# Performance work log

Measured on AMD Instinct MI355X. Metric: run time of the kernel, lower is better.

Reference implementation:

```python
import jax, jax.numpy as jnp
import numpy as np

N = 250_000   # total instances
D = 128       # instance latent dim
F = 512       # raw instance feature dim
B = 5000      # number of bags


def setup_inputs() -> dict:
    key = jax.random.key(0)
    ks = jax.random.split(key, 7)
    z_ins = jax.random.normal(ks[0], (N, D), dtype=jnp.float32)
    bag_idx = jnp.sort(jax.random.randint(ks[1], (N,), 0, B, dtype=jnp.int32))
    bag_instances = jax.random.normal(ks[2], (N, F), dtype=jnp.float32)
    instance_mu = jax.random.normal(ks[3], (N, D), dtype=jnp.float32)
    instance_std = jax.random.uniform(ks[4], (N, D), dtype=jnp.float32)
    W = jax.random.normal(ks[5], (D, 1), dtype=jnp.float32) * 0.05
    b = jnp.zeros((1,), dtype=jnp.float32)
    return {"z_ins": z_ins, "bag_idx": bag_idx, "bag_instances": bag_instances,
            "instance_mu": instance_mu, "instance_std": instance_std,
            "W": W, "b": b}


def reference(z_ins, bag_idx, bag_instances, instance_mu, instance_std, W, b):
    # loc_ins = fc_ins(z_ins): [N, 1]
    loc_ins = z_ins @ W + b
    loc = loc_ins[:, 0]  # [N]

    # Segmented max over bags; argmax gather (first max index, matching torch.max).
    seg_max = jax.ops.segment_max(loc, bag_idx, num_segments=B)          # [B]
    is_max = loc == seg_max[bag_idx]                                     # [N]
    cand = jnp.where(is_max, jnp.arange(N, dtype=jnp.int32), N)
    arg = jax.ops.segment_min(cand, bag_idx, num_segments=B)            # [B]
    empty = arg >= N                                                     # bags with no instances stay zero
    arg_c = jnp.minimum(arg, N - 1)

    def gather(x):
        return jnp.where(empty[:, None], jnp.zeros((), x.dtype), x[arg_c])

    M = gather(loc_ins)                       # [B, 1]
    max_z_ins = gather(z_ins)                 # [B, D]
    max_instances = gather(bag_instances)     # [B, F]
    max_instances_mu = gather(instance_mu)    # [B, D]
    max_instances_std = gather(instance_std)  # [B, D]
    return (M, max_instances, max_z_ins, loc_ins, max_instances_mu, max_instances_std)
```

## Files before the change

kernel.cpp:

```cpp
#include <hip/hip_runtime.h>

#define DD 128
#define FF 512
#define BAGS 5000

__device__ __forceinline__ unsigned fkey(float f) {
    unsigned u = __float_as_uint(f);
    return (u & 0x80000000u) ? ~u : (u | 0x80000000u);
}
__device__ __forceinline__ float fkey_inv(unsigned k) {
    unsigned u = (k & 0x80000000u) ? (k & 0x7FFFFFFFu) : ~k;
    return __uint_as_float(u);
}

__global__ __launch_bounds__(256) void loc_seg_kernel(
    const float* __restrict__ z, const int* __restrict__ bag,
    const float* __restrict__ W, const float* __restrict__ b,
    float* __restrict__ loc, unsigned long long* __restrict__ packed, int N)
{
    int tid  = threadIdx.x;
    int lane = tid & 63;
    int wave = tid >> 6;
    int o    = lane & 7;
    int rowslot = lane >> 3;

    long long rowbase = (long long)blockIdx.x * 256 + wave * 64;

    float4 wk[4];
    #pragma unroll
    for (int j = 0; j < 4; ++j) wk[j] = ((const float4*)W)[o + 8 * j];
    float bb = b[0];

    float myloc = 0.f;
    #pragma unroll
    for (int t = 0; t < 8; ++t) {
        long long row = rowbase + t * 8 + rowslot;
        float4 acc = make_float4(0.f, 0.f, 0.f, 0.f);
        if (row < N) {
            const float4* zr = (const float4*)(z + row * DD);
            #pragma unroll
            for (int j = 0; j < 4; ++j) {
                float4 zv = zr[o + 8 * j];
                acc.x = fmaf(zv.x, wk[j].x, acc.x);
                acc.y = fmaf(zv.y, wk[j].y, acc.y);
                acc.z = fmaf(zv.z, wk[j].z, acc.z);
                acc.w = fmaf(zv.w, wk[j].w, acc.w);
            }
        }
        float sd = (acc.x + acc.y) + (acc.z + acc.w);
        sd += __shfl_xor(sd, 1, 64);
        sd += __shfl_xor(sd, 2, 64);
        sd += __shfl_xor(sd, 4, 64);
        float v = __shfl(sd, (lane & 7) * 8, 64);
        if (t == (lane >> 3)) myloc = v;
    }

    long long row = rowbase + lane;
    bool valid = row < N;
    myloc += bb;
    int bl = -1;
    unsigned long long key = 0ull;
    if (valid) {
        loc[row] = myloc;
        bl = bag[row];
        key = ((unsigned long long)fkey(myloc) << 32) | (unsigned)(N - 1 - (int)row);
    }
    #pragma unroll
    for (int off = 1; off <= 32; off <<= 1) {
        int src = lane + off;
        int clamped = src < 64 ? src : lane;
        unsigned long long okey = __shfl(key, clamped, 64);
        int obag = __shfl(bl, clamped, 64);
        if (src < 64 && obag == bl && okey > key) key = okey;
    }
    int pb = __shfl(bl, lane > 0 ? lane - 1 : 0, 64);
    bool head = valid && (lane == 0 || pb != bl);
    if (head) atomicMax(&packed[bl], key);
}

__global__ __launch_bounds__(256) void gather_kernel(
    const float* __restrict__ z, const float* __restrict__ inst,
    const float* __restrict__ mu, const float* __restrict__ stdv,
    const unsigned long long* __restrict__ packed,
    float* __restrict__ oM, float* __restrict__ oInst, float* __restrict__ oZ,
    float* __restrict__ oMu, float* __restrict__ oStd, int N)
{
    int bagi = blockIdx.x;
    unsigned long long p = packed[bagi];
    bool empty = (p == 0ull);
    long long ac = empty ? 0 : (long long)(N - 1 - (int)(unsigned)(p & 0xFFFFFFFFull));
    const float4 zero4 = make_float4(0.f, 0.f, 0.f, 0.f);
    int t = threadIdx.x;
    if (t < 128) {
        float4 v = empty ? zero4 : ((const float4*)(inst + ac * FF))[t];
        ((float4*)(oInst + (long long)bagi * FF))[t] = v;
    } else if (t < 160) {
        int k = t - 128;
        float4 v = empty ? zero4 : ((const float4*)(z + ac * DD))[k];
        ((float4*)(oZ + (long long)bagi * DD))[k] = v;
    } else if (t < 192) {
        int k = t - 160;
        float4 v = empty ? zero4 : ((const float4*)(mu + ac * DD))[k];
        ((float4*)(oMu + (long long)bagi * DD))[k] = v;
    } else if (t < 224) {
        int k = t - 192;
        float4 v = empty ? zero4 : ((const float4*)(stdv + ac * DD))[k];
        ((float4*)(oStd + (long long)bagi * DD))[k] = v;
    } else if (t == 224) {
        oM[bagi] = empty ? 0.f : fkey_inv((unsigned)(p >> 32));
    }
}

extern "C" void kernel_launch(void* const* d_in, const int* in_sizes, int n_in,
                              void* d_out, int out_size, void* d_ws, size_t ws_size,
                              hipStream_t stream) {
    const float* z    = (const float*)d_in[0];
    const int*   bag  = (const int*)d_in[1];
    const float* inst = (const float*)d_in[2];
    const float* mu   = (const float*)d_in[3];
    const float* stdv = (const float*)d_in[4];
    const float* W    = (const float*)d_in[5];
    const float* b    = (const float*)d_in[6];
    int N = in_sizes[1];

    float* out = (float*)d_out;
    long long off_inst = BAGS;
    long long off_z    = off_inst + (long long)BAGS * FF;
    long long off_loc  = off_z    + (long long)BAGS * DD;
    long long off_mu   = off_loc  + N;
    long long off_std  = off_mu   + (long long)BAGS * DD;

    unsigned long long* packed = (unsigned long long*)d_ws;
    float* loc = out + off_loc;

    hipMemsetAsync(packed, 0, BAGS * sizeof(unsigned long long), stream);
    int blocks = (N + 255) / 256;
    loc_seg_kernel<<<blocks, 256, 0, stream>>>(z, bag, W, b, loc, packed, N);
    gather_kernel<<<BAGS, 256, 0, stream>>>(z, inst, mu, stdv, packed,
                                            out, out + off_inst, out + off_z,
                                            out + off_mu, out + off_std, N);
}
```

Baseline: 40.24 us.

## Fuse segment argmax and gather into a single kernel with last-arriver completion

Merges the loc/segment-max kernel and the gather kernel into one launch. Bags that lie wholly inside a block are reduced in shared memory and gathered immediately. Bags that span blocks are tracked with atomic start/end/count counters, so the last contributing block does the gather. Empty bags are zeroed inline by the thread that sees the gap in bag indices. This removes the second launch and the global round trip on the argmax keys, but adds atomics, fences and serial per-lane fallback paths.

```diff
diff --git a/kernel.cpp b/kernel.cpp
--- a/kernel.cpp
+++ b/kernel.cpp
@@ -3,6 +3,7 @@
 #define DD 128
 #define FF 512
 #define BAGS 5000
+#define TASK_CAP 32
 
 __device__ __forceinline__ unsigned fkey(float f) {
     unsigned u = __float_as_uint(f);
@@ -13,28 +14,72 @@
     return __uint_as_float(u);
 }
 
-__global__ __launch_bounds__(256) void loc_seg_kernel(
+__device__ void zero_bag(int bg, float* oM, float* oInst, float* oZ,
+                         float* oMu, float* oStd) {
+    oM[bg] = 0.f;
+    const float4 z4 = make_float4(0.f, 0.f, 0.f, 0.f);
+    float4* pi = (float4*)(oInst + (long long)bg * FF);
+    for (int k = 0; k < FF / 4; ++k) pi[k] = z4;
+    float4* pz = (float4*)(oZ + (long long)bg * DD);
+    float4* pm = (float4*)(oMu + (long long)bg * DD);
+    float4* ps = (float4*)(oStd + (long long)bg * DD);
+    for (int k = 0; k < DD / 4; ++k) { pz[k] = z4; pm[k] = z4; ps[k] = z4; }
+}
+
+__device__ void lane_gather(int bg, unsigned long long p, int N,
+                            const float* z, const float* inst, const float* mu,
+                            const float* stdv, float* oM, float* oInst,
+                            float* oZ, float* oMu, float* oStd) {
+    long long ac = N - 1 - (int)(unsigned)(p & 0xFFFFFFFFull);
+    oM[bg] = fkey_inv((unsigned)(p >> 32));
+    for (int k = 0; k < FF; ++k) oInst[(long long)bg * FF + k] = inst[ac * FF + k];
+    for (int k = 0; k < DD; ++k) {
+        oZ[(long long)bg * DD + k]  = z[ac * DD + k];
+        oMu[(long long)bg * DD + k] = mu[ac * DD + k];
+        oStd[(long long)bg * DD + k] = stdv[ac * DD + k];
+    }
+}
+
+__global__ __launch_bounds__(256) void fused_kernel(
     const float* __restrict__ z, const int* __restrict__ bag,
-    const float* __restrict__ W, const float* __restrict__ b,
-    float* __restrict__ loc, unsigned long long* __restrict__ packed, int N)
+    const float* __restrict__ inst, const float* __restrict__ mu,
+    const float* __restrict__ stdv, const float* __restrict__ W,
+    const float* __restrict__ bptr,
+    float* __restrict__ oM, float* __restrict__ oInst, float* __restrict__ oZ,
+    float* __restrict__ oMu, float* __restrict__ oStd, float* __restrict__ loc,
+    unsigned long long* __restrict__ packed, unsigned* __restrict__ bagstart,
+    unsigned* __restrict__ bagend, unsigned* __restrict__ done, int N)
 {
+    __shared__ unsigned long long keyA[256];
+    __shared__ int bagA[256];
+    __shared__ int s_prev, s_next, s_ntask;
+    __shared__ int taskBag[TASK_CAP];
+    __shared__ unsigned long long taskKey[TASK_CAP];
+
     int tid  = threadIdx.x;
     int lane = tid & 63;
     int wave = tid >> 6;
-    int o    = lane & 7;
+    long long rowbase = (long long)blockIdx.x * 256;
+
+    if (tid == 0) {
+        s_prev = (rowbase > 0) ? bag[rowbase - 1] : -1;
+        long long nr = rowbase + 256;
+        s_next = (nr < N) ? bag[nr] : BAGS;
+        s_ntask = 0;
+    }
+
+    int o = lane & 7;
     int rowslot = lane >> 3;
-
-    long long rowbase = (long long)blockIdx.x * 256 + wave * 64;
-
+    long long wbase = rowbase + (long long)wave * 64;
     float4 wk[4];
     #pragma unroll
     for (int j = 0; j < 4; ++j) wk[j] = ((const float4*)W)[o + 8 * j];
-    float bb = b[0];
+    float bb = bptr[0];
 
     float myloc = 0.f;
     #pragma unroll
     for (int t = 0; t < 8; ++t) {
-        long long row = rowbase + t * 8 + rowslot;
+        long long row = wbase + t * 8 + rowslot;
         float4 acc = make_float4(0.f, 0.f, 0.f, 0.f);
         if (row < N) {
             const float4* zr = (const float4*)(z + row * DD);
@@ -55,59 +100,102 @@
         if (t == (lane >> 3)) myloc = v;
     }
 
-    long long row = rowbase + lane;
-    bool valid = row < N;
+    long long myrow = wbase + lane;
+    bool valid = myrow < N;
     myloc += bb;
-    int bl = -1;
-    unsigned long long key = 0ull;
+    int mybag = BAGS;
+    unsigned long long mykey = 0ull;
     if (valid) {
-        loc[row] = myloc;
-        bl = bag[row];
-        key = ((unsigned long long)fkey(myloc) << 32) | (unsigned)(N - 1 - (int)row);
-    }
+        loc[myrow] = myloc;
+        mybag = bag[myrow];
+        mykey = ((unsigned long long)fkey(myloc) << 32) | (unsigned)(N - 1 - (int)myrow);
+    }
+
     #pragma unroll
     for (int off = 1; off <= 32; off <<= 1) {
         int src = lane + off;
-        int clamped = src < 64 ? src : lane;
-        unsigned long long okey = __shfl(key, clamped, 64);
-        int obag = __shfl(bl, clamped, 64);
-        if (src < 64 && obag == bl && okey > key) key = okey;
-    }
-    int pb = __shfl(bl, lane > 0 ? lane - 1 : 0, 64);
-    bool head = valid && (lane == 0 || pb != bl);
-    if (head) atomicMax(&packed[bl], key);
-}
-
-__global__ __launch_bounds__(256) void gather_kernel(
-    const float* __restrict__ z, const float* __restrict__ inst,
-    const float* __restrict__ mu, const float* __restrict__ stdv,
-    const unsigned long long* __restrict__ packed,
-    float* __restrict__ oM, float* __restrict__ oInst, float* __restrict__ oZ,
-    float* __restrict__ oMu, float* __restrict__ oStd, int N)
-{
-    int bagi = blockIdx.x;
-    unsigned long long p = packed[bagi];
-    bool empty = (p == 0ull);
-    long long ac = empty ? 0 : (long long)(N - 1 - (int)(unsigned)(p & 0xFFFFFFFFull));
-    const float4 zero4 = make_float4(0.f, 0.f, 0.f, 0.f);
-    int t = threadIdx.x;
-    if (t < 128) {
-        float4 v = empty ? zero4 : ((const float4*)(inst + ac * FF))[t];
-        ((float4*)(oInst + (long long)bagi * FF))[t] = v;
-    } else if (t < 160) {
-        int k = t - 128;
-        float4 v = empty ? zero4 : ((const float4*)(z + ac * DD))[k];
-        ((float4*)(oZ + (long long)bagi * DD))[k] = v;
-    } else if (t < 192) {
-        int k = t - 160;
-        float4 v = empty ? zero4 : ((const float4*)(mu + ac * DD))[k];
-        ((float4*)(oMu + (long long)bagi * DD))[k] = v;
-    } else if (t < 224) {
-        int k = t - 192;
-        float4 v = empty ? zero4 : ((const float4*)(stdv + ac * DD))[k];
-        ((float4*)(oStd + (long long)bagi * DD))[k] = v;
-    } else if (t == 224) {
-        oM[bagi] = empty ? 0.f : fkey_inv((unsigned)(p >> 32));
+        int cl = src < 64 ? src : lane;
+        unsigned long long ok = __shfl(mykey, cl, 64);
+        int ob = __shfl(mybag, cl, 64);
+        if (src < 64 && ob == mybag && ok > mykey) mykey = ok;
+    }
+    keyA[tid] = mykey;
+    bagA[tid] = mybag;
+    __syncthreads();
+
+    int pb = (tid == 0) ? s_prev : bagA[tid - 1];
+    bool rep = valid && (tid == 0 || pb != mybag);
+
+    if (rep) {
+        for (int w2 = wave + 1; w2 < 4; ++w2) {
+            if (bagA[w2 * 64] != mybag) break;
+            unsigned long long ok = keyA[w2 * 64];
+            if (ok > mykey) mykey = ok;
+        }
+    }
+
+    {
+        int hi = (mybag < BAGS ? mybag : BAGS) - 1;
+        for (int bg = pb + 1; bg <= hi; ++bg)
+            zero_bag(bg, oM, oInst, oZ, oMu, oStd);
+        if (valid && tid == 255 && rowbase + 256 >= N && mybag < BAGS - 1)
+            for (int bg = mybag + 1; bg < BAGS; ++bg)
+                zero_bag(bg, oM, oInst, oZ, oMu, oStd);
+    }
+
+    if (rep) {
+        int lastbagblk = bagA[255];
+        bool gfirst = (tid > 0) || (mybag != s_prev);
+        bool reaches_end = (mybag == lastbagblk);
+        bool glast = !reaches_end || (s_next != mybag);
+
+        if (gfirst && glast) {
+            int idx = atomicAdd(&s_ntask, 1);
+            if (idx < TASK_CAP) { taskBag[idx] = mybag; taskKey[idx] = mykey; }
+            else lane_gather(mybag, mykey, N, z, inst, mu, stdv, oM, oInst, oZ, oMu, oStd);
+        } else {
+            int t2 = tid;
+            while (t2 + 1 < 256 && bagA[t2 + 1] == mybag) ++t2;
+            int C = t2 - tid + 1;
+            if (gfirst) atomicMax(&bagstart[mybag], (unsigned)(N - (int)(rowbase + tid)));
+            if (glast)  atomicMax(&bagend[mybag],   (unsigned)(rowbase + t2 + 1));
+            atomicMax(&packed[mybag], mykey);
+            __threadfence();
+            unsigned total = atomicAdd(&done[mybag], (unsigned)C) + (unsigned)C;
+            __threadfence();
+            unsigned bs = atomicMax(&bagstart[mybag], 0u);
+            unsigned be = atomicMax(&bagend[mybag], 0u);
+            if (bs != 0u && be != 0u &&
+                (long long)total == (long long)be + (long long)bs - (long long)N) {
+                unsigned long long K = atomicMax(&packed[mybag], 0ull);
+                int idx = atomicAdd(&s_ntask, 1);
+                if (idx < TASK_CAP) { taskBag[idx] = mybag; taskKey[idx] = K; }
+                else lane_gather(mybag, K, N, z, inst, mu, stdv, oM, oInst, oZ, oMu, oStd);
+            }
+        }
+    }
+    __syncthreads();
+
+    int nt = s_ntask; if (nt > TASK_CAP) nt = TASK_CAP;
+    for (int q = 0; q < nt; ++q) {
+        int bg = taskBag[q];
+        unsigned long long p = taskKey[q];
+        long long ac = N - 1 - (int)(unsigned)(p & 0xFFFFFFFFull);
+        int t = tid;
+        if (t < 128) {
+            ((float4*)(oInst + (long long)bg * FF))[t] = ((const float4*)(inst + ac * FF))[t];
+        } else if (t < 160) {
+            int k = t - 128;
+            ((float4*)(oZ + (long long)bg * DD))[k] = ((const float4*)(z + ac * DD))[k];
+        } else if (t < 192) {
+            int k = t - 160;
+            ((float4*)(oMu + (long long)bg * DD))[k] = ((const float4*)(mu + ac * DD))[k];
+        } else if (t < 224) {
+            int k = t - 192;
+            ((float4*)(oStd + (long long)bg * DD))[k] = ((const float4*)(stdv + ac * DD))[k];
+        } else if (t == 224) {
+            oM[bg] = fkey_inv((unsigned)(p >> 32));
+        }
     }
 }
 
@@ -131,12 +219,15 @@
     long long off_std  = off_mu   + (long long)BAGS * DD;
 
     unsigned long long* packed = (unsigned long long*)d_ws;
-    float* loc = out + off_loc;
-
-    hipMemsetAsync(packed, 0, BAGS * sizeof(unsigned long long), stream);
+    unsigned* bagstart = (unsigned*)((char*)d_ws + BAGS * 8);
+    unsigned* bagend   = (unsigned*)((char*)d_ws + BAGS * 8 + BAGS * 4);
+    unsigned* done     = (unsigned*)((char*)d_ws + BAGS * 8 + BAGS * 8);
+
+    hipMemsetAsync(d_ws, 0, BAGS * 20, stream);
     int blocks = (N + 255) / 256;
-    loc_seg_kernel<<<blocks, 256, 0, stream>>>(z, bag, W, b, loc, packed, N);
-    gather_kernel<<<BAGS, 256, 0, stream>>>(z, inst, mu, stdv, packed,
-                                            out, out + off_inst, out + off_z,
-                                            out + off_mu, out + off_std, N);
-}
+    fused_kernel<<<blocks, 256, 0, stream>>>(
+        z, bag, inst, mu, stdv, W, b,
+        out, out + off_inst, out + off_z, out + off_mu, out + off_std,
+        out + off_loc,
+        packed, bagstart, bagend, done, N);
+}
```

Measured after the change: 123.0 us. +205.7%, slower.

## Replace atomic segment max with segment start offsets and per-bag reduction

Applied to the files above, without the earlier changes.

The first kernel no longer runs a wave-level segmented scan and atomicMax on packed keys. It writes segment start offsets from boundaries in the sorted bag indices. The gather kernel then reads each bag's range, reduces the argmax over loc with one wave, and copies the rows. This drops the memset launch and the atomics, at the cost of re-reading loc per bag and a serial wave reduction before the copy. It relies on bag_idx being sorted.

```diff
diff --git a/kernel.cpp b/kernel.cpp
--- a/kernel.cpp
+++ b/kernel.cpp
@@ -13,10 +13,10 @@
     return __uint_as_float(u);
 }
 
-__global__ __launch_bounds__(256) void loc_seg_kernel(
+__global__ __launch_bounds__(256) void loc_kernel(
     const float* __restrict__ z, const int* __restrict__ bag,
     const float* __restrict__ W, const float* __restrict__ b,
-    float* __restrict__ loc, unsigned long long* __restrict__ packed, int N)
+    float* __restrict__ loc, int* __restrict__ start, int N)
 {
     int tid  = threadIdx.x;
     int lane = tid & 63;
@@ -24,7 +24,7 @@
     int o    = lane & 7;
     int rowslot = lane >> 3;
 
-    long long rowbase = (long long)blockIdx.x * 256 + wave * 64;
+    long long wbase = (long long)blockIdx.x * 256 + wave * 64;
 
     float4 wk[4];
     #pragma unroll
@@ -34,7 +34,7 @@
     float myloc = 0.f;
     #pragma unroll
     for (int t = 0; t < 8; ++t) {
-        long long row = rowbase + t * 8 + rowslot;
+        long long row = wbase + t * 8 + rowslot;
         float4 acc = make_float4(0.f, 0.f, 0.f, 0.f);
         if (row < N) {
             const float4* zr = (const float4*)(z + row * DD);
@@ -55,42 +55,61 @@
         if (t == (lane >> 3)) myloc = v;
     }
 
-    long long row = rowbase + lane;
+    long long row = wbase + lane;
     bool valid = row < N;
-    myloc += bb;
-    int bl = -1;
-    unsigned long long key = 0ull;
     if (valid) {
-        loc[row] = myloc;
-        bl = bag[row];
-        key = ((unsigned long long)fkey(myloc) << 32) | (unsigned)(N - 1 - (int)row);
+        loc[row] = myloc + bb;
+        int cb = bag[row];
+        int pb = __shfl_up(cb, 1, 64);
+        if (lane == 0) pb = (row > 0) ? bag[row - 1] : -1;
+        if (row == 0 || cb != pb) {
+            for (int bg = (row == 0 ? 0 : pb + 1); bg <= cb; ++bg)
+                start[bg] = (int)row;
+        }
+        if (row == N - 1) {
+            for (int bg = cb + 1; bg <= BAGS; ++bg)
+                start[bg] = N;
+        }
     }
-    #pragma unroll
-    for (int off = 1; off <= 32; off <<= 1) {
-        int src = lane + off;
-        int clamped = src < 64 ? src : lane;
-        unsigned long long okey = __shfl(key, clamped, 64);
-        int obag = __shfl(bl, clamped, 64);
-        if (src < 64 && obag == bl && okey > key) key = okey;
-    }
-    int pb = __shfl(bl, lane > 0 ? lane - 1 : 0, 64);
-    bool head = valid && (lane == 0 || pb != bl);
-    if (head) atomicMax(&packed[bl], key);
 }
 
 __global__ __launch_bounds__(256) void gather_kernel(
     const float* __restrict__ z, const float* __restrict__ inst,
     const float* __restrict__ mu, const float* __restrict__ stdv,
-    const unsigned long long* __restrict__ packed,
+    const float* __restrict__ loc, const int* __restrict__ start,
     float* __restrict__ oM, float* __restrict__ oInst, float* __restrict__ oZ,
     float* __restrict__ oMu, float* __restrict__ oStd, int N)
 {
+    __shared__ unsigned long long s_res;
+    __shared__ int s_se[2];
+
     int bagi = blockIdx.x;
-    unsigned long long p = packed[bagi];
-    bool empty = (p == 0ull);
+    int tid = threadIdx.x;
+    if (tid < 2) s_se[tid] = start[bagi + tid];
+    __syncthreads();
+    int s = s_se[0], e = s_se[1];
+
+    if (tid < 64) {
+        unsigned long long best = 0ull;
+        for (int r = s + tid; r < e; r += 64) {
+            unsigned long long key =
+                ((unsigned long long)fkey(loc[r]) << 32) | (unsigned)(N - 1 - r);
+            if (key > best) best = key;
+        }
+        #pragma unroll
+        for (int off = 32; off >= 1; off >>= 1) {
+            unsigned long long o = __shfl_xor(best, off, 64);
+            if (o > best) best = o;
+        }
+        if (tid == 0) s_res = best;
+    }
+    __syncthreads();
+
+    unsigned long long p = s_res;
+    bool empty = (e <= s);
     long long ac = empty ? 0 : (long long)(N - 1 - (int)(unsigned)(p & 0xFFFFFFFFull));
     const float4 zero4 = make_float4(0.f, 0.f, 0.f, 0.f);
-    int t = threadIdx.x;
+    int t = tid;
     if (t < 128) {
         float4 v = empty ? zero4 : ((const float4*)(inst + ac * FF))[t];
         ((float4*)(oInst + (long long)bagi * FF))[t] = v;
@@ -130,13 +149,12 @@
     long long off_mu   = off_loc  + N;
     long long off_std  = off_mu   + (long long)BAGS * DD;
 
-    unsigned long long* packed = (unsigned long long*)d_ws;
+    int* startArr = (int*)d_ws;
     float* loc = out + off_loc;
 
-    hipMemsetAsync(packed, 0, BAGS * sizeof(unsigned long long), stream);
     int blocks = (N + 255) / 256;
-    loc_seg_kernel<<<blocks, 256, 0, stream>>>(z, bag, W, b, loc, packed, N);
-    gather_kernel<<<BAGS, 256, 0, stream>>>(z, inst, mu, stdv, packed,
+    loc_kernel<<<blocks, 256, 0, stream>>>(z, bag, W, b, loc, startArr, N);
+    gather_kernel<<<BAGS, 256, 0, stream>>>(z, inst, mu, stdv, loc, startArr,
                                             out, out + off_inst, out + off_z,
                                             out + off_mu, out + off_std, N);
 }
```

After: 37.73 us. 6.2% less time.
